# Kernel tuning notes

Measured on AMD Instinct MI355X. Metric: run time of the kernel, lower is better.

## Reference

```python
import jax, jax.numpy as jnp
import numpy as np

N = 262144
D = 1024
H = 512
B = 512  # number of bags / segments


def setup_inputs() -> dict:
    key = jax.random.key(0)
    k1, k2, k3, k4, k5 = jax.random.split(key, 5)
    x = jax.random.normal(k1, (N, D), dtype=jnp.float32)
    batch = jnp.sort(jax.random.randint(k2, (N,), 0, B, dtype=jnp.int64))
    s1 = 1.0 / np.sqrt(D)
    s3 = 1.0 / np.sqrt(H)
    W1 = jax.random.uniform(k3, (H, D), dtype=jnp.float32, minval=-s1, maxval=s1)
    W2 = jax.random.uniform(k4, (H, D), dtype=jnp.float32, minval=-s1, maxval=s1)
    W3 = jax.random.uniform(k5, (1, H), dtype=jnp.float32, minval=-s3, maxval=s3)
    return {"x": x, "batch": batch, "W1": W1, "W2": W2, "W3": W3}


def reference(x, batch, W1, W2, W3):
    # gated attention logits: tanh(x W1^T) * softmax_over_h(x W2^T) -> W3
    ux = jnp.tanh(x @ W1.T)                       # (n, h)
    vx = jax.nn.softmax(x @ W2.T, axis=1)         # (n, h), Softmax(dim=1)
    alpha = (ux * vx) @ W3.T                      # (n, 1)

    # segment-wise stable softmax over instances within each bag
    a = alpha[:, 0]                               # (n,)
    seg_max = jax.ops.segment_max(a, batch, num_segments=B)   # (B,)
    e = jnp.exp(a - seg_max[batch])               # (n,)
    seg_sum = jax.ops.segment_sum(e, batch, num_segments=B)   # (B,)
    w = e / seg_sum[batch]                        # (n,)

    # weighted segment add-pool: (B, d)
    z = jax.ops.segment_sum(x * w[:, None], batch, num_segments=B)
    return z
```

## Files before the change

### kernel.cpp

```cpp
#include <hip/hip_runtime.h>
#include <stdint.h>

#define N_ROWS 262144
#define D_DIM  1024
#define H_DIM  512
#define N_SEG  512

typedef __attribute__((ext_vector_type(4)))  float  f32x4;
typedef __attribute__((ext_vector_type(8)))  __bf16 bf16x8;
typedef __attribute__((ext_vector_type(8)))  unsigned short u16x8;

static __device__ __forceinline__ unsigned short c2bf(float f) {
  union { __bf16 b; unsigned short u; } c; c.b = (__bf16)f; return c.u;
}
static __device__ __forceinline__ float fast_tanh(float u) {
  return 1.0f - 2.0f / (__expf(2.0f * u) + 1.0f);
}

__global__ void cvt_w(const float* __restrict__ W1, const float* __restrict__ W2,
                      unsigned short* __restrict__ wbf) {
  int gid = blockIdx.x * 256 + threadIdx.x;
  int l   = gid & 63;
  int cfi = (gid >> 6) & 15;
  int kt  = (gid >> 10) & 31;
  int hs  = gid >> 15;
  int c   = (cfi << 4) + (l & 15);
  int h   = (hs << 7) + (c >> 1);
  int k0  = (kt << 5) + ((l >> 4) << 3);
  const float* src = ((c & 1) ? W2 : W1) + h * 1024 + k0;
  f32x4 f0 = *(const f32x4*)src;
  f32x4 f1 = *(const f32x4*)(src + 4);
  u16x8 v;
  v[0]=c2bf(f0[0]); v[1]=c2bf(f0[1]); v[2]=c2bf(f0[2]); v[3]=c2bf(f0[3]);
  v[4]=c2bf(f1[0]); v[5]=c2bf(f1[1]); v[6]=c2bf(f1[2]); v[7]=c2bf(f1[3]);
  *(u16x8*)(wbf + (size_t)gid * 8) = v;
}

#define MF(A, B, C) __builtin_amdgcn_mfma_f32_16x16x32_bf16((A), (B), (C), 0, 0, 0)

#define STAGEB(KT, BOFF) do { \
  __builtin_amdgcn_global_load_lds( \
    (const __attribute__((address_space(1))) void*)(wsrc + ((uint32_t)(KT) << 13)), \
    (__attribute__((address_space(3))) void*)(lds + (BOFF) + (wid << 11)), 16, 0, 0); \
  __builtin_amdgcn_global_load_lds( \
    (const __attribute__((address_space(1))) void*)(wsrc + ((uint32_t)(KT) << 13) + 512), \
    (__attribute__((address_space(3))) void*)(lds + (BOFF) + (wid << 11) + 1024), 16, 0, 0); \
} while (0)

#define ALOADP(KT) do { \
  pA0 = *(const f32x4*)(xsrc0 + ((KT) << 5));     pA1 = *(const f32x4*)(xsrc0 + ((KT) << 5) + 4); \
  pB0 = *(const f32x4*)(xsrc1 + ((KT) << 5));     pB1 = *(const f32x4*)(xsrc1 + ((KT) << 5) + 4); \
} while (0)
#define ALOADQ(KT) do { \
  qA0 = *(const f32x4*)(xsrc0 + ((KT) << 5));     qA1 = *(const f32x4*)(xsrc0 + ((KT) << 5) + 4); \
  qB0 = *(const f32x4*)(xsrc1 + ((KT) << 5));     qB1 = *(const f32x4*)(xsrc1 + ((KT) << 5) + 4); \
} while (0)

#define PACKSET(BOFF, A0, A1, B0, B1) do { \
  u16x8 va, vb; \
  va[0]=c2bf(A0[0]); va[1]=c2bf(A0[1]); va[2]=c2bf(A0[2]); va[3]=c2bf(A0[3]); \
  va[4]=c2bf(A1[0]); va[5]=c2bf(A1[1]); va[6]=c2bf(A1[2]); va[7]=c2bf(A1[3]); \
  vb[0]=c2bf(B0[0]); vb[1]=c2bf(B0[1]); vb[2]=c2bf(B0[2]); vb[3]=c2bf(B0[3]); \
  vb[4]=c2bf(B1[0]); vb[5]=c2bf(B1[1]); vb[6]=c2bf(B1[2]); vb[7]=c2bf(B1[3]); \
  *(u16x8*)(lds + (BOFF) + (tid << 4)) = va; \
  *(u16x8*)(lds + (BOFF) + 8192 + (tid << 4)) = vb; \
} while (0)

#define COMPUTE(PAR) do { \
  bf16x8 bf_[4], af[8]; \
  _Pragma("unroll") \
  for (int fc = 0; fc < 4; ++fc) \
    bf_[fc] = *(const bf16x8*)(lds + 32768 + ((PAR) << 14) + (((cg << 2) + fc) << 10) + (lane << 4)); \
  _Pragma("unroll") \
  for (int fr = 0; fr < 8; ++fr) \
    af[fr] = *(const bf16x8*)(lds + ((PAR) << 14) + (((rg << 3) + fr) << 10) + (lane << 4)); \
  __builtin_amdgcn_s_setprio(1); \
  _Pragma("unroll") \
  for (int fr = 0; fr < 8; ++fr) \
    _Pragma("unroll") \
    for (int fc = 0; fc < 4; ++fc) \
      acc[fr][fc] = MF(af[fr], bf_[fc], acc[fr][fc]); \
  __builtin_amdgcn_s_setprio(0); \
} while (0)

#define BAR2() do { \
  asm volatile("s_waitcnt vmcnt(2) lgkmcnt(0)" ::: "memory"); \
  __builtin_amdgcn_s_barrier(); \
} while (0)
#define BAR0() do { \
  asm volatile("s_waitcnt vmcnt(0) lgkmcnt(0)" ::: "memory"); \
  __builtin_amdgcn_s_barrier(); \
} while (0)

__launch_bounds__(512, 2)
__global__ void alpha_kernel(const float* __restrict__ x,
                             const unsigned short* __restrict__ wbf,
                             const float* __restrict__ W3,
                             float* __restrict__ pm, float* __restrict__ ps,
                             float* __restrict__ pn)
{
  __shared__ unsigned char lds[65536];
  const int tid  = threadIdx.x;
  const int lane = tid & 63;
  const int wid  = tid >> 6;
  const int rg   = wid >> 2;
  const int cg   = wid & 3;
  const int l15  = lane & 15;
  const int lg   = lane >> 4;
  const int bid  = blockIdx.x;
  const int rt   = ((bid >> 5) << 3) + (bid & 7);
  const int hs   = (bid >> 3) & 3;
  const int row0 = rt << 8;

  const int s0r = ((tid >> 6) << 4) + (tid & 15);
  const int s0k = ((tid >> 4) & 3) << 3;
  const float* xsrc0 = x + (size_t)(row0 + s0r) * 1024 + s0k;
  const float* xsrc1 = xsrc0 + (size_t)128 * 1024;

  const unsigned short* wsrc = wbf + ((uint32_t)hs << 18) + ((uint32_t)wid << 10) + ((uint32_t)lane << 3);

  f32x4 acc[8][4];
  #pragma unroll
  for (int fr = 0; fr < 8; ++fr)
    #pragma unroll
    for (int fc = 0; fc < 4; ++fc) acc[fr][fc] = (f32x4){0.f, 0.f, 0.f, 0.f};

  f32x4 pA0, pA1, pB0, pB1;
  f32x4 qA0, qA1, qB0, qB1;

  STAGEB(0, 32768);
  ALOADP(0);
  ALOADQ(1);
  PACKSET(0, pA0, pA1, pB0, pB1);
  BAR2();

  #pragma unroll 1
  for (int kt = 0; kt < 30; kt += 2) {
    STAGEB(kt + 1, 49152);
    ALOADP(kt + 2);
    COMPUTE(0);
    PACKSET(16384, qA0, qA1, qB0, qB1);
    BAR2();
    STAGEB(kt + 2, 32768);
    ALOADQ(kt + 3);
    COMPUTE(1);
    PACKSET(0, pA0, pA1, pB0, pB1);
    BAR2();
  }

  STAGEB(31, 49152);
  COMPUTE(0);
  PACKSET(16384, qA0, qA1, qB0, qB1);
  BAR0();
  COMPUTE(1);

  float w3v[4];
  #pragma unroll
  for (int fc = 0; fc < 4; ++fc)
    w3v[fc] = W3[(hs << 7) + (((cg << 6) + (fc << 4) + l15) >> 1)];

  float* pmb = (float*)(lds);
  float* psb = pmb + 1024;
  float* pnb = psb + 1024;

  #pragma unroll
  for (int fr = 0; fr < 8; ++fr) {
    f32x4 mv, sv, nv;
    #pragma unroll
    for (int j = 0; j < 4; ++j) {
      float g0 = fast_tanh(acc[fr][0][j]) * w3v[0];
      float g1 = fast_tanh(acc[fr][1][j]) * w3v[1];
      float g2 = fast_tanh(acc[fr][2][j]) * w3v[2];
      float g3 = fast_tanh(acc[fr][3][j]) * w3v[3];
      float gs0 = __shfl_xor(g0, 1);
      float gs1 = __shfl_xor(g1, 1);
      float gs2 = __shfl_xor(g2, 1);
      float gs3 = __shfl_xor(g3, 1);
      float mj = fmaxf(fmaxf(acc[fr][0][j], acc[fr][1][j]),
                       fmaxf(acc[fr][2][j], acc[fr][3][j]));
      mj = fmaxf(mj, __shfl_xor(mj, 2));
      mj = fmaxf(mj, __shfl_xor(mj, 4));
      mj = fmaxf(mj, __shfl_xor(mj, 8));
      float p0 = __expf(acc[fr][0][j] - mj);
      float p1 = __expf(acc[fr][1][j] - mj);
      float p2 = __expf(acc[fr][2][j] - mj);
      float p3 = __expf(acc[fr][3][j] - mj);
      float sj = p0 + p1 + p2 + p3;
      float nj = gs0 * p0 + gs1 * p1 + gs2 * p2 + gs3 * p3;
      sj += __shfl_xor(sj, 2); nj += __shfl_xor(nj, 2);
      sj += __shfl_xor(sj, 4); nj += __shfl_xor(nj, 4);
      sj += __shfl_xor(sj, 8); nj += __shfl_xor(nj, 8);
      mv[j] = mj; sv[j] = sj; nv[j] = nj;
    }
    if (l15 == 1) {
      int idx = (cg << 8) + (rg << 7) + (fr << 4) + (lg << 2);
      *(f32x4*)&pmb[idx] = mv;
      *(f32x4*)&psb[idx] = sv;
      *(f32x4*)&pnb[idx] = nv;
    }
  }
  __syncthreads();
  if (tid < 256) {
    float m0 = pmb[tid], m1 = pmb[256 + tid], m2 = pmb[512 + tid], m3 = pmb[768 + tid];
    float M = fmaxf(fmaxf(m0, m1), fmaxf(m2, m3));
    float e0 = __expf(m0 - M), e1 = __expf(m1 - M), e2 = __expf(m2 - M), e3 = __expf(m3 - M);
    float S  = psb[tid]*e0 + psb[256+tid]*e1 + psb[512+tid]*e2 + psb[768+tid]*e3;
    float Nn = pnb[tid]*e0 + pnb[256+tid]*e1 + pnb[512+tid]*e2 + pnb[768+tid]*e3;
    size_t r = (size_t)(row0 + tid);
    pm[r * 4 + hs] = M;
    ps[r * 4 + hs] = S;
    pn[r * 4 + hs] = Nn;
  }
}

__global__ void combine_a(const float* __restrict__ pm, const float* __restrict__ ps,
                          const float* __restrict__ pn, float* __restrict__ a) {
  size_t r = (size_t)blockIdx.x * 256 + threadIdx.x;
  float M = -3.4e38f;
  #pragma unroll
  for (int s = 0; s < 4; ++s) M = fmaxf(M, pm[r * 4 + s]);
  float S = 0.f, Nn = 0.f;
  #pragma unroll
  for (int s = 0; s < 4; ++s) {
    float e = __expf(pm[r * 4 + s] - M);
    S  += ps[r * 4 + s] * e;
    Nn += pn[r * 4 + s] * e;
  }
  a[r] = Nn / S;
}

static __device__ __forceinline__ int lower_bound(const int* __restrict__ batch, int key) {
  int lo = 0, hi = N_ROWS;
  while (lo < hi) { int mid = (lo + hi) >> 1; if (batch[mid] < key) lo = mid + 1; else hi = mid; }
  return lo;
}

__global__ void seg_kernel(const float* __restrict__ a, const int* __restrict__ batch,
                           float* __restrict__ w) {
  __shared__ float sm[8];
  int b = blockIdx.x;
  int start = lower_bound(batch, b);
  int end   = lower_bound(batch, b + 1);
  int tid = threadIdx.x;

  float m = -3.4e38f;
  for (int i = start + tid; i < end; i += 256) m = fmaxf(m, a[i]);
  for (int d = 1; d < 64; d <<= 1) m = fmaxf(m, __shfl_xor(m, d));
  if ((tid & 63) == 0) sm[tid >> 6] = m;
  __syncthreads();
  m = fmaxf(fmaxf(sm[0], sm[1]), fmaxf(sm[2], sm[3]));

  float s = 0.f;
  for (int i = start + tid; i < end; i += 256) s += __expf(a[i] - m);
  for (int d = 1; d < 64; d <<= 1) s += __shfl_xor(s, d);
  if ((tid & 63) == 0) sm[4 + (tid >> 6)] = s;
  __syncthreads();
  s = sm[4] + sm[5] + sm[6] + sm[7];

  float rinv = 1.0f / s;
  for (int i = start + tid; i < end; i += 256) w[i] = __expf(a[i] - m) * rinv;
}

__global__ void z_kernel(const float* __restrict__ x, const float* __restrict__ w,
                         const int* __restrict__ batch, float* __restrict__ z) {
  int b = blockIdx.x >> 2, part = blockIdx.x & 3;
  int start = lower_bound(batch, b);
  int end   = lower_bound(batch, b + 1);
  int len = end - start;
  int ps = start + ((len * part) >> 2);
  int pe = start + ((len * (part + 1)) >> 2);
  int col = threadIdx.x << 2;

  f32x4 acc = (f32x4){0.f, 0.f, 0.f, 0.f};
  for (int i = ps; i < pe; ++i) {
    f32x4 xv = *(const f32x4*)(x + ((size_t)i << 10) + col);
    float wi = w[i];
    acc += xv * wi;
  }
  float* zp = z + ((size_t)b << 10) + col;
  atomicAdd(zp + 0, acc[0]);
  atomicAdd(zp + 1, acc[1]);
  atomicAdd(zp + 2, acc[2]);
  atomicAdd(zp + 3, acc[3]);
}

extern "C" void kernel_launch(void* const* d_in, const int* in_sizes, int n_in,
                              void* d_out, int out_size, void* d_ws, size_t ws_size,
                              hipStream_t stream) {
  const float* x     = (const float*)d_in[0];
  const int*   batch = (const int*)d_in[1];
  const float* W1    = (const float*)d_in[2];
  const float* W2    = (const float*)d_in[3];
  const float* W3    = (const float*)d_in[4];
  float* z = (float*)d_out;

  unsigned short* wbf = (unsigned short*)d_ws;
  float* a  = (float*)((char*)d_ws + (2u << 20));
  float* w  = (float*)((char*)d_ws + (3u << 20));
  float* pm = (float*)((char*)d_ws + (4u << 20));
  float* ps = (float*)((char*)d_ws + (8u << 20));
  float* pn = (float*)((char*)d_ws + (12u << 20));

  (void)hipMemsetAsync(d_out, 0, (size_t)N_SEG * D_DIM * sizeof(float), stream);

  cvt_w<<<512, 256, 0, stream>>>(W1, W2, wbf);

  alpha_kernel<<<4096, 512, 0, stream>>>(x, wbf, W3, pm, ps, pn);

  combine_a<<<N_ROWS / 256, 256, 0, stream>>>(pm, ps, pn, a);

  seg_kernel<<<N_SEG, 256, 0, stream>>>(a, batch, w);

  z_kernel<<<N_SEG * 4, 256, 0, stream>>>(x, w, batch, z);
}
```

Baseline: 1.249 ms.

## Halve alpha GEMM row tile to 128 to raise occupancy

Result: faster. 1.035 ms (-17.1%).

```diff
diff --git a/kernel.cpp b/kernel.cpp
--- a/kernel.cpp
+++ b/kernel.cpp
@@ -47,36 +47,29 @@
     (__attribute__((address_space(3))) void*)(lds + (BOFF) + (wid << 11) + 1024), 16, 0, 0); \
 } while (0)
 
-#define ALOADP(KT) do { \
-  pA0 = *(const f32x4*)(xsrc0 + ((KT) << 5));     pA1 = *(const f32x4*)(xsrc0 + ((KT) << 5) + 4); \
-  pB0 = *(const f32x4*)(xsrc1 + ((KT) << 5));     pB1 = *(const f32x4*)(xsrc1 + ((KT) << 5) + 4); \
-} while (0)
-#define ALOADQ(KT) do { \
-  qA0 = *(const f32x4*)(xsrc0 + ((KT) << 5));     qA1 = *(const f32x4*)(xsrc0 + ((KT) << 5) + 4); \
-  qB0 = *(const f32x4*)(xsrc1 + ((KT) << 5));     qB1 = *(const f32x4*)(xsrc1 + ((KT) << 5) + 4); \
-} while (0)
-
-#define PACKSET(BOFF, A0, A1, B0, B1) do { \
-  u16x8 va, vb; \
-  va[0]=c2bf(A0[0]); va[1]=c2bf(A0[1]); va[2]=c2bf(A0[2]); va[3]=c2bf(A0[3]); \
-  va[4]=c2bf(A1[0]); va[5]=c2bf(A1[1]); va[6]=c2bf(A1[2]); va[7]=c2bf(A1[3]); \
-  vb[0]=c2bf(B0[0]); vb[1]=c2bf(B0[1]); vb[2]=c2bf(B0[2]); vb[3]=c2bf(B0[3]); \
-  vb[4]=c2bf(B1[0]); vb[5]=c2bf(B1[1]); vb[6]=c2bf(B1[2]); vb[7]=c2bf(B1[3]); \
+#define ALOAD(KT) do { \
+  rA0 = *(const f32x4*)(xsrc + ((KT) << 5)); \
+  rA1 = *(const f32x4*)(xsrc + ((KT) << 5) + 4); \
+} while (0)
+
+#define PACKA(BOFF) do { \
+  u16x8 va; \
+  va[0]=c2bf(rA0[0]); va[1]=c2bf(rA0[1]); va[2]=c2bf(rA0[2]); va[3]=c2bf(rA0[3]); \
+  va[4]=c2bf(rA1[0]); va[5]=c2bf(rA1[1]); va[6]=c2bf(rA1[2]); va[7]=c2bf(rA1[3]); \
   *(u16x8*)(lds + (BOFF) + (tid << 4)) = va; \
-  *(u16x8*)(lds + (BOFF) + 8192 + (tid << 4)) = vb; \
-} while (0)
-
-#define COMPUTE(PAR) do { \
-  bf16x8 bf_[4], af[8]; \
+} while (0)
+
+#define COMPUTE(ABUF, BBUF) do { \
+  bf16x8 bf_[4], af[4]; \
   _Pragma("unroll") \
   for (int fc = 0; fc < 4; ++fc) \
-    bf_[fc] = *(const bf16x8*)(lds + 32768 + ((PAR) << 14) + (((cg << 2) + fc) << 10) + (lane << 4)); \
+    bf_[fc] = *(const bf16x8*)(lds + (BBUF) + (((cg << 2) + fc) << 10) + (lane << 4)); \
   _Pragma("unroll") \
-  for (int fr = 0; fr < 8; ++fr) \
-    af[fr] = *(const bf16x8*)(lds + ((PAR) << 14) + (((rg << 3) + fr) << 10) + (lane << 4)); \
+  for (int fr = 0; fr < 4; ++fr) \
+    af[fr] = *(const bf16x8*)(lds + (ABUF) + (((rg << 2) + fr) << 10) + (lane << 4)); \
   __builtin_amdgcn_s_setprio(1); \
   _Pragma("unroll") \
-  for (int fr = 0; fr < 8; ++fr) \
+  for (int fr = 0; fr < 4; ++fr) \
     _Pragma("unroll") \
     for (int fc = 0; fc < 4; ++fc) \
       acc[fr][fc] = MF(af[fr], bf_[fc], acc[fr][fc]); \
@@ -92,14 +85,14 @@
   __builtin_amdgcn_s_barrier(); \
 } while (0)
 
-__launch_bounds__(512, 2)
+__launch_bounds__(512, 4)
 __global__ void alpha_kernel(const float* __restrict__ x,
                              const unsigned short* __restrict__ wbf,
                              const float* __restrict__ W3,
                              float* __restrict__ pm, float* __restrict__ ps,
                              float* __restrict__ pn)
 {
-  __shared__ unsigned char lds[65536];
+  __shared__ unsigned char lds[49152];
   const int tid  = threadIdx.x;
   const int lane = tid & 63;
   const int wid  = tid >> 6;
@@ -110,49 +103,45 @@
   const int bid  = blockIdx.x;
   const int rt   = ((bid >> 5) << 3) + (bid & 7);
   const int hs   = (bid >> 3) & 3;
-  const int row0 = rt << 8;
-
-  const int s0r = ((tid >> 6) << 4) + (tid & 15);
-  const int s0k = ((tid >> 4) & 3) << 3;
-  const float* xsrc0 = x + (size_t)(row0 + s0r) * 1024 + s0k;
-  const float* xsrc1 = xsrc0 + (size_t)128 * 1024;
+  const int row0 = rt << 7;
+
+  const float* xsrc = x + (size_t)(row0 + ((tid >> 6) << 4) + (tid & 15)) * 1024
+                        + (((tid >> 4) & 3) << 3);
 
   const unsigned short* wsrc = wbf + ((uint32_t)hs << 18) + ((uint32_t)wid << 10) + ((uint32_t)lane << 3);
 
-  f32x4 acc[8][4];
-  #pragma unroll
-  for (int fr = 0; fr < 8; ++fr)
+  f32x4 acc[4][4];
+  #pragma unroll
+  for (int fr = 0; fr < 4; ++fr)
     #pragma unroll
     for (int fc = 0; fc < 4; ++fc) acc[fr][fc] = (f32x4){0.f, 0.f, 0.f, 0.f};
 
-  f32x4 pA0, pA1, pB0, pB1;
-  f32x4 qA0, qA1, qB0, qB1;
-
-  STAGEB(0, 32768);
-  ALOADP(0);
-  ALOADQ(1);
-  PACKSET(0, pA0, pA1, pB0, pB1);
+  f32x4 rA0, rA1;
+
+  STAGEB(0, 16384);
+  ALOAD(0);
+  PACKA(0);
+  ALOAD(1);
   BAR2();
 
   #pragma unroll 1
   for (int kt = 0; kt < 30; kt += 2) {
-    STAGEB(kt + 1, 49152);
-    ALOADP(kt + 2);
-    COMPUTE(0);
-    PACKSET(16384, qA0, qA1, qB0, qB1);
+    STAGEB(kt + 1, 32768);
+    COMPUTE(0, 16384);
+    PACKA(8192);
+    ALOAD(kt + 2);
     BAR2();
-    STAGEB(kt + 2, 32768);
-    ALOADQ(kt + 3);
-    COMPUTE(1);
-    PACKSET(0, pA0, pA1, pB0, pB1);
+    STAGEB(kt + 2, 16384);
+    COMPUTE(8192, 32768);
+    PACKA(0);
+    ALOAD(kt + 3);
     BAR2();
   }
-
-  STAGEB(31, 49152);
-  COMPUTE(0);
-  PACKSET(16384, qA0, qA1, qB0, qB1);
+  STAGEB(31, 32768);
+  COMPUTE(0, 16384);
+  PACKA(8192);
   BAR0();
-  COMPUTE(1);
+  COMPUTE(8192, 32768);
 
   float w3v[4];
   #pragma unroll
@@ -160,11 +149,11 @@
     w3v[fc] = W3[(hs << 7) + (((cg << 6) + (fc << 4) + l15) >> 1)];
 
   float* pmb = (float*)(lds);
-  float* psb = pmb + 1024;
-  float* pnb = psb + 1024;
-
-  #pragma unroll
-  for (int fr = 0; fr < 8; ++fr) {
+  float* psb = pmb + 512;
+  float* pnb = psb + 512;
+
+  #pragma unroll
+  for (int fr = 0; fr < 4; ++fr) {
     f32x4 mv, sv, nv;
     #pragma unroll
     for (int j = 0; j < 4; ++j) {
@@ -193,19 +182,19 @@
       mv[j] = mj; sv[j] = sj; nv[j] = nj;
     }
     if (l15 == 1) {
-      int idx = (cg << 8) + (rg << 7) + (fr << 4) + (lg << 2);
+      int idx = (cg << 7) + (rg << 6) + (fr << 4) + (lg << 2);
       *(f32x4*)&pmb[idx] = mv;
       *(f32x4*)&psb[idx] = sv;
       *(f32x4*)&pnb[idx] = nv;
     }
   }
   __syncthreads();
-  if (tid < 256) {
-    float m0 = pmb[tid], m1 = pmb[256 + tid], m2 = pmb[512 + tid], m3 = pmb[768 + tid];
+  if (tid < 128) {
+    float m0 = pmb[tid], m1 = pmb[128 + tid], m2 = pmb[256 + tid], m3 = pmb[384 + tid];
     float M = fmaxf(fmaxf(m0, m1), fmaxf(m2, m3));
     float e0 = __expf(m0 - M), e1 = __expf(m1 - M), e2 = __expf(m2 - M), e3 = __expf(m3 - M);
-    float S  = psb[tid]*e0 + psb[256+tid]*e1 + psb[512+tid]*e2 + psb[768+tid]*e3;
-    float Nn = pnb[tid]*e0 + pnb[256+tid]*e1 + pnb[512+tid]*e2 + pnb[768+tid]*e3;
+    float S  = psb[tid]*e0 + psb[128+tid]*e1 + psb[256+tid]*e2 + psb[384+tid]*e3;
+    float Nn = pnb[tid]*e0 + pnb[128+tid]*e1 + pnb[256+tid]*e2 + pnb[384+tid]*e3;
     size_t r = (size_t)(row0 + tid);
     pm[r * 4 + hs] = M;
     ps[r * 4 + hs] = S;
@@ -305,7 +294,7 @@
 
   cvt_w<<<512, 256, 0, stream>>>(W1, W2, wbf);
 
-  alpha_kernel<<<4096, 512, 0, stream>>>(x, wbf, W3, pm, ps, pn);
+  alpha_kernel<<<8192, 512, 0, stream>>>(x, wbf, W3, pm, ps, pn);
 
   combine_a<<<N_ROWS / 256, 256, 0, stream>>>(pm, ps, pn, a);
 
```

## Split GEMM main loop into four interleaved phases with finer barriers

Applied to the files above, without the earlier changes.

Result: slower. 1.350 ms (+8.1%).

```diff
diff --git a/kernel.cpp b/kernel.cpp
--- a/kernel.cpp
+++ b/kernel.cpp
@@ -47,48 +47,67 @@
     (__attribute__((address_space(3))) void*)(lds + (BOFF) + (wid << 11) + 1024), 16, 0, 0); \
 } while (0)
 
-#define ALOADP(KT) do { \
-  pA0 = *(const f32x4*)(xsrc0 + ((KT) << 5));     pA1 = *(const f32x4*)(xsrc0 + ((KT) << 5) + 4); \
-  pB0 = *(const f32x4*)(xsrc1 + ((KT) << 5));     pB1 = *(const f32x4*)(xsrc1 + ((KT) << 5) + 4); \
-} while (0)
-#define ALOADQ(KT) do { \
-  qA0 = *(const f32x4*)(xsrc0 + ((KT) << 5));     qA1 = *(const f32x4*)(xsrc0 + ((KT) << 5) + 4); \
-  qB0 = *(const f32x4*)(xsrc1 + ((KT) << 5));     qB1 = *(const f32x4*)(xsrc1 + ((KT) << 5) + 4); \
-} while (0)
-
-#define PACKSET(BOFF, A0, A1, B0, B1) do { \
+#define ALOAD(KT) do { \
+  rA0 = *(const f32x4*)(xsrc0 + ((KT) << 5)); rA1 = *(const f32x4*)(xsrc0 + ((KT) << 5) + 4); \
+  rB0 = *(const f32x4*)(xsrc1 + ((KT) << 5)); rB1 = *(const f32x4*)(xsrc1 + ((KT) << 5) + 4); \
+} while (0)
+
+#define PACKA(BOFF) do { \
   u16x8 va, vb; \
-  va[0]=c2bf(A0[0]); va[1]=c2bf(A0[1]); va[2]=c2bf(A0[2]); va[3]=c2bf(A0[3]); \
-  va[4]=c2bf(A1[0]); va[5]=c2bf(A1[1]); va[6]=c2bf(A1[2]); va[7]=c2bf(A1[3]); \
-  vb[0]=c2bf(B0[0]); vb[1]=c2bf(B0[1]); vb[2]=c2bf(B0[2]); vb[3]=c2bf(B0[3]); \
-  vb[4]=c2bf(B1[0]); vb[5]=c2bf(B1[1]); vb[6]=c2bf(B1[2]); vb[7]=c2bf(B1[3]); \
+  va[0]=c2bf(rA0[0]); va[1]=c2bf(rA0[1]); va[2]=c2bf(rA0[2]); va[3]=c2bf(rA0[3]); \
+  va[4]=c2bf(rA1[0]); va[5]=c2bf(rA1[1]); va[6]=c2bf(rA1[2]); va[7]=c2bf(rA1[3]); \
+  vb[0]=c2bf(rB0[0]); vb[1]=c2bf(rB0[1]); vb[2]=c2bf(rB0[2]); vb[3]=c2bf(rB0[3]); \
+  vb[4]=c2bf(rB1[0]); vb[5]=c2bf(rB1[1]); vb[6]=c2bf(rB1[2]); vb[7]=c2bf(rB1[3]); \
   *(u16x8*)(lds + (BOFF) + (tid << 4)) = va; \
   *(u16x8*)(lds + (BOFF) + 8192 + (tid << 4)) = vb; \
 } while (0)
 
-#define COMPUTE(PAR) do { \
-  bf16x8 bf_[4], af[8]; \
-  _Pragma("unroll") \
-  for (int fc = 0; fc < 4; ++fc) \
-    bf_[fc] = *(const bf16x8*)(lds + 32768 + ((PAR) << 14) + (((cg << 2) + fc) << 10) + (lane << 4)); \
-  _Pragma("unroll") \
-  for (int fr = 0; fr < 8; ++fr) \
-    af[fr] = *(const bf16x8*)(lds + ((PAR) << 14) + (((rg << 3) + fr) << 10) + (lane << 4)); \
+#define LDB(BUF, FC) (*(const bf16x8*)(lds + (BUF) + (((cg << 2) + (FC)) << 10) + (lane << 4)))
+#define LDA(BUF, FR) (*(const bf16x8*)(lds + (BUF) + (((rg << 3) + (FR)) << 10) + (lane << 4)))
+
+#define MFQ(I0, A0_, A1_, A2_, A3_, B0_, B1_) do { \
   __builtin_amdgcn_s_setprio(1); \
-  _Pragma("unroll") \
-  for (int fr = 0; fr < 8; ++fr) \
-    _Pragma("unroll") \
-    for (int fc = 0; fc < 4; ++fc) \
-      acc[fr][fc] = MF(af[fr], bf_[fc], acc[fr][fc]); \
+  acc[I0+0][0] = MF(A0_, B0_, acc[I0+0][0]); acc[I0+0][1] = MF(A0_, B1_, acc[I0+0][1]); \
+  acc[I0+1][0] = MF(A1_, B0_, acc[I0+1][0]); acc[I0+1][1] = MF(A1_, B1_, acc[I0+1][1]); \
+  acc[I0+2][0] = MF(A2_, B0_, acc[I0+2][0]); acc[I0+2][1] = MF(A2_, B1_, acc[I0+2][1]); \
+  acc[I0+3][0] = MF(A3_, B0_, acc[I0+3][0]); acc[I0+3][1] = MF(A3_, B1_, acc[I0+3][1]); \
   __builtin_amdgcn_s_setprio(0); \
 } while (0)
-
-#define BAR2() do { \
-  asm volatile("s_waitcnt vmcnt(2) lgkmcnt(0)" ::: "memory"); \
-  __builtin_amdgcn_s_barrier(); \
-} while (0)
-#define BAR0() do { \
-  asm volatile("s_waitcnt vmcnt(0) lgkmcnt(0)" ::: "memory"); \
+#define MFQ2(I0, A0_, A1_, A2_, A3_, B2_, B3_) do { \
+  __builtin_amdgcn_s_setprio(1); \
+  acc[I0+0][2] = MF(A0_, B2_, acc[I0+0][2]); acc[I0+0][3] = MF(A0_, B3_, acc[I0+0][3]); \
+  acc[I0+1][2] = MF(A1_, B2_, acc[I0+1][2]); acc[I0+1][3] = MF(A1_, B3_, acc[I0+1][3]); \
+  acc[I0+2][2] = MF(A2_, B2_, acc[I0+2][2]); acc[I0+2][3] = MF(A2_, B3_, acc[I0+2][3]); \
+  acc[I0+3][2] = MF(A3_, B2_, acc[I0+3][2]); acc[I0+3][3] = MF(A3_, B3_, acc[I0+3][3]); \
+  __builtin_amdgcn_s_setprio(0); \
+} while (0)
+
+#define PHASE(AB, BB, AO, BO, KT, DOALOAD) do { \
+   \
+  bf16x8 a0 = LDA(AB, 0), a1 = LDA(AB, 1), a2 = LDA(AB, 2), a3 = LDA(AB, 3); \
+  bf16x8 b0 = LDB(BB, 0), b1 = LDB(BB, 1); \
+  STAGEB((KT) + 1, BO); \
+  __builtin_amdgcn_s_barrier(); \
+  asm volatile("s_waitcnt lgkmcnt(0)" ::: "memory"); \
+  MFQ(0, a0, a1, a2, a3, b0, b1); \
+  __builtin_amdgcn_s_barrier(); \
+   \
+  bf16x8 b2 = LDB(BB, 2), b3 = LDB(BB, 3); \
+  PACKA(AO); \
+  __builtin_amdgcn_s_barrier(); \
+  asm volatile("s_waitcnt lgkmcnt(0)" ::: "memory"); \
+  MFQ2(0, a0, a1, a2, a3, b2, b3); \
+  __builtin_amdgcn_s_barrier(); \
+   \
+  bf16x8 a4 = LDA(AB, 4), a5 = LDA(AB, 5), a6 = LDA(AB, 6), a7 = LDA(AB, 7); \
+  if (DOALOAD) ALOAD((KT) + 2); \
+  __builtin_amdgcn_s_barrier(); \
+  asm volatile("s_waitcnt lgkmcnt(0)" ::: "memory"); \
+  MFQ(4, a4, a5, a6, a7, b0, b1); \
+  __builtin_amdgcn_s_barrier(); \
+   \
+  MFQ2(4, a4, a5, a6, a7, b2, b3); \
+  asm volatile("s_waitcnt vmcnt(4)" ::: "memory"); \
   __builtin_amdgcn_s_barrier(); \
 } while (0)
 
@@ -125,34 +144,33 @@
     #pragma unroll
     for (int fc = 0; fc < 4; ++fc) acc[fr][fc] = (f32x4){0.f, 0.f, 0.f, 0.f};
 
-  f32x4 pA0, pA1, pB0, pB1;
-  f32x4 qA0, qA1, qB0, qB1;
+  f32x4 rA0, rA1, rB0, rB1;
 
   STAGEB(0, 32768);
-  ALOADP(0);
-  ALOADQ(1);
-  PACKSET(0, pA0, pA1, pB0, pB1);
-  BAR2();
+  ALOAD(0);
+  PACKA(0);
+  ALOAD(1);
+  asm volatile("s_waitcnt vmcnt(4) lgkmcnt(0)" ::: "memory");
+  __builtin_amdgcn_s_barrier();
 
   #pragma unroll 1
   for (int kt = 0; kt < 30; kt += 2) {
-    STAGEB(kt + 1, 49152);
-    ALOADP(kt + 2);
-    COMPUTE(0);
-    PACKSET(16384, qA0, qA1, qB0, qB1);
-    BAR2();
-    STAGEB(kt + 2, 32768);
-    ALOADQ(kt + 3);
-    COMPUTE(1);
-    PACKSET(0, pA0, pA1, pB0, pB1);
-    BAR2();
-  }
-
-  STAGEB(31, 49152);
-  COMPUTE(0);
-  PACKSET(16384, qA0, qA1, qB0, qB1);
-  BAR0();
-  COMPUTE(1);
+    PHASE(0,     32768, 16384, 49152, kt,     1);
+    PHASE(16384, 49152, 0,     32768, kt + 1, 1);
+  }
+  PHASE(0, 32768, 16384, 49152, 30, 0);
+  asm volatile("s_waitcnt vmcnt(0) lgkmcnt(0)" ::: "memory");
+  __builtin_amdgcn_s_barrier();
+  {
+    bf16x8 a0 = LDA(16384, 0), a1 = LDA(16384, 1), a2 = LDA(16384, 2), a3 = LDA(16384, 3);
+    bf16x8 a4 = LDA(16384, 4), a5 = LDA(16384, 5), a6 = LDA(16384, 6), a7 = LDA(16384, 7);
+    bf16x8 b0 = LDB(49152, 0), b1 = LDB(49152, 1), b2 = LDB(49152, 2), b3 = LDB(49152, 3);
+    MFQ(0, a0, a1, a2, a3, b0, b1);
+    MFQ2(0, a0, a1, a2, a3, b2, b3);
+    MFQ(4, a4, a5, a6, a7, b0, b1);
+    MFQ2(4, a4, a5, a6, a7, b2, b3);
+  }
+  __builtin_amdgcn_s_barrier();
 
   float w3v[4];
   #pragma unroll
```
